# Kernel optimization log

Measured on AMD Instinct MI355X. Metric: run time of the kernel, lower is better.

Reference implementation:

```python
import jax, jax.numpy as jnp
import numpy as np

B, N, T, IN_DIM, OUT_DIM = 16, 500, 12, 2, 2
H, D, K, NH, NBLOCKS, T_OUT, GDEP = 64, 64, 10, 24, 2, 12, 2
H2 = 2 * H


def setup_inputs():
    key = jax.random.key(0)
    ks = iter(jax.random.split(key, 64))

    def rn(shape, s=1.0):
        return jax.random.normal(next(ks), shape, dtype=jnp.float32) * s

    def z(*shape):
        return jnp.zeros(shape, jnp.float32)

    sI = 1.0 / np.sqrt(IN_DIM)
    sH = 1.0 / np.sqrt(H)
    sH2 = 1.0 / np.sqrt(H2)
    sD = 1.0 / np.sqrt(D)
    adj = jax.random.uniform(next(ks), (N, N), dtype=jnp.float32)
    inp = {
        'x': rn((B, N, T, IN_DIM)),
        'weather': rn((B, T, 4)),
        'geo_adj': adj / adj.sum(1, keepdims=True),
        'fcx_W': rn((IN_DIM, H), sI), 'fcx_b': z(H),
        'env_cb': rn((K, D)), 'nodes_cb': rn((N, D)),
        'w_v': rn((D, K), sD), 'w_k': rn((D, D), sD), 'w_q': rn((D, D), sD),
        'core_W': rn((H, H * H), sH), 'core_b': z(H * H),
        'tcnN_Win': rn((K, H2, H2), sH2), 'tcnN_bin': z(K, H2),
        'tcnN_Wf': rn((K, NBLOCKS, 2, H2, H2), sH2), 'tcnN_bf': z(K, NBLOCKS, H2),
        'tcnN_Wg': rn((K, NBLOCKS, 2, H2, H2), sH2), 'tcnN_bg': z(K, NBLOCKS, H2),
        'tcnN_Wout': rn((K, H2, H), sH2), 'tcnN_bout': z(K, H),
        'tcnP_Win': rn((K, H2, H2), sH2), 'tcnP_bin': z(K, H2),
        'tcnP_Wf': rn((K, NBLOCKS, 2, H2, H2), sH2), 'tcnP_bf': z(K, NBLOCKS, H2),
        'tcnP_Wg': rn((K, NBLOCKS, 2, H2, H2), sH2), 'tcnP_bg': z(K, NBLOCKS, H2),
        'tcnP_Wout': rn((K, H2, H), sH2), 'tcnP_bout': z(K, H),
        'bn1_g': jnp.ones((H,), jnp.float32), 'bn1_b': z(H),
        'bnP_g': jnp.ones((H,), jnp.float32), 'bnP_b': z(H),
        'gcn1_W': rn((H, H), sH), 'gcn1_b': z(H),
        'gcn2_W': rn((H, H), sH), 'gcn2_b': z(H),
        'gcnp_W': rn((H, H), sH), 'gcnp_b': z(H),
        'nv_p1': rn((2 * NH, H)), 'nv_p2': rn((N, H)), 'nv_p3': rn((N, H)),
        'nv_pk': rn((H, H, H), sH),
        'out_W1': rn((T_OUT, H, 100), sH), 'out_b1': z(T_OUT, 100),
        'out_W2': rn((T_OUT, 100, OUT_DIM), 0.1), 'out_b2': z(T_OUT, OUT_DIM),
        't_pos': jax.random.randint(next(ks), (B, T, 2), 0, 7),
        'ind': jax.random.randint(next(ks), (B, T, 2), 0, 7),
    }
    return inp


def _tstep_emb(t, dim):
    half = dim // 2
    freqs = jnp.exp(-jnp.log(10000.0) * jnp.arange(half, dtype=jnp.float32) / half)
    a = t.astype(jnp.float32)[:, None] * freqs[None]
    return jnp.concatenate([jnp.cos(a), jnp.sin(a)], -1)


def _conv2(h, W, b, d):
    # causal kernel-2 dilated conv over time: h [B,N,T,C], W [2,C,Co] -> [B,N,T-d,Co]
    return (jnp.einsum('bntc,co->bnto', h[:, :, :-d], W[0])
            + jnp.einsum('bntc,co->bnto', h[:, :, d:], W[1]) + b)


def _tcn(xin, Win, bin_, Wf, bf, Wg, bg, Wout, bout):
    # gated dilated TCN (Graph-WaveNet style), per node over time
    h = jnp.einsum('bntc,co->bnto', xin, Win) + bin_
    for l in range(Wf.shape[0]):
        d = 2 ** l
        f = jnp.tanh(_conv2(h, Wf[l], bf[l], d))
        g = jax.nn.sigmoid(_conv2(h, Wg[l], bg[l], d))
        h = f * g + h[:, :, d:, :]
    return jnp.einsum('bntc,ch->bnth', h, Wout) + bout


def _bn(h, g, b):
    # BatchNorm1d over channels, stats over (batch, nodes); training mode
    mu = h.mean((0, 1))
    var = h.var((0, 1))
    return g * (h - mu) * jax.lax.rsqrt(var + 1e-5) + b


def _gcn(h, adj, W, b):
    # multi-hop diffusion: sum_{k=0..GDEP} A^k h, then linear
    eq = 'nm,bmh->bnh' if adj.ndim == 2 else 'bnm,bmh->bnh'
    acc, zt = h, h
    for _ in range(GDEP):
        zt = jnp.einsum(eq, adj, zt)
        acc = acc + zt
    return jnp.einsum('bnh,ho->bno', acc, W) + b


def _forward(x, weather, geo_adj, fcx_W, fcx_b, env_cb, nodes_cb, w_v, w_k, w_q,
             core_W, core_b,
             tcnN_Win, tcnN_bin, tcnN_Wf, tcnN_bf, tcnN_Wg, tcnN_bg, tcnN_Wout, tcnN_bout,
             tcnP_Win, tcnP_bin, tcnP_Wf, tcnP_bf, tcnP_Wg, tcnP_bg, tcnP_Wout, tcnP_bout,
             bn1_g, bn1_b, bnP_g, bnP_b, gcn1_W, gcn1_b, gcn2_W, gcn2_b, gcnp_W, gcnp_b,
             nv_p1, nv_p2, nv_p3, nv_pk, out_W1, out_b1, out_W2, out_b2, t_pos, ind):
    scale = 1.0 / jnp.sqrt(jnp.float32(D))
    ind_p = jnp.where(ind[:, :, 0] <= 4, ind[:, :, 1], NH - 1 + ind[:, :, 1])
    tp = jnp.where(t_pos[:, :, 0] <= 4, t_pos[:, :, 1], NH - 1 + t_pos[:, :, 1])
    t_emb = _tstep_emb(tp.reshape(-1), H).reshape(B, T, H)

    # codebook attention -> hard cluster assignment (gumbel softmax, straight-through)
    mat_v = env_cb @ w_v
    mat_k = env_cb @ w_k
    mat_q = nodes_cb @ w_q
    scores = jax.nn.softmax((mat_q @ mat_k.T) * scale, axis=1)
    logits = scores @ mat_v                                   # [N,K]
    gn = jax.random.gumbel(jax.random.key(42), logits.shape, dtype=logits.dtype)
    y_soft = jax.nn.softmax(logits + gn, axis=1)
    hard = jax.nn.one_hot(jnp.argmax(y_soft, axis=1), K, dtype=y_soft.dtype)
    mask = y_soft + jax.lax.stop_gradient(hard - y_soft)      # [N,K] one-hot fwd

    x_emb = jnp.einsum('bnti,ih->bnth', x, fcx_W) + fcx_b
    total_x = jnp.concatenate(
        [x_emb, jnp.broadcast_to(t_emb[:, None], (B, N, T, H))], -1)  # [B,N,T,2H]

    unbias = jnp.zeros((B, N, H), total_x.dtype)
    h_prev = jnp.zeros((B, N, H), total_x.dtype)
    for i in range(K):  # small fixed cluster count
        m = mask[:, i]
        xm = total_x * m[None, :, None, None]
        hn = _tcn(xm[:, :, 1:], tcnN_Win[i], tcnN_bin[i], tcnN_Wf[i], tcnN_bf[i],
                  tcnN_Wg[i], tcnN_bg[i], tcnN_Wout[i], tcnN_bout[i])[:, :, 0, :]
        hp = _tcn(xm[:, :, :-1], tcnP_Win[i], tcnP_bin[i], tcnP_Wf[i], tcnP_bf[i],
                  tcnP_Wg[i], tcnP_bg[i], tcnP_Wout[i], tcnP_bout[i])[:, :, 0, :]
        unbias = unbias + m[None, :, None] * hn
        h_prev = h_prev + m[None, :, None] * hp

    unbias = _bn(unbias, bn1_g, bn1_b)
    h_prev = _bn(h_prev, bnP_g, bnP_b)

    h1 = _gcn(h_prev, geo_adj, gcn1_W, gcn1_b)
    core = (t_emb[:, T - 1] @ core_W + core_b).reshape(B, H, H)
    causal = jax.nn.softmax(jnp.einsum('bnh,bhk,bmk->bnm', unbias, core, h_prev), axis=-1)
    h2 = _gcn(unbias, causal, gcn2_W, gcn2_b)

    te = nv_p1[ind_p[:, -(T - 1)]]                            # [B,H]
    adp = jnp.einsum('ai,ijk->ajk', te, nv_pk)
    adp = jnp.einsum('bj,ajk->abk', nv_p2, adp)
    adp = jnp.einsum('ck,abk->abc', nv_p3, adp)
    adp = jax.nn.softmax(jax.nn.relu(adp), axis=2)            # [B,N,N]
    h3 = _gcn(unbias, adp, gcnp_W, gcnp_b)

    cur_h = h1 + h2 + h3
    hmid = jax.nn.elu(jnp.einsum('bnh,thf->bntf', cur_h, out_W1) + out_b1)
    return jnp.einsum('bntf,tfo->bnto', hmid, out_W2) + out_b2  # [B,N,T_OUT,OUT_DIM]


def reference(x, weather, geo_adj, fcx_W, fcx_b, env_cb, nodes_cb, w_v, w_k, w_q,
              core_W, core_b,
              tcnN_Win, tcnN_bin, tcnN_Wf, tcnN_bf, tcnN_Wg, tcnN_bg, tcnN_Wout, tcnN_bout,
              tcnP_Win, tcnP_bin, tcnP_Wf, tcnP_bf, tcnP_Wg, tcnP_bg, tcnP_Wout, tcnP_bout,
              bn1_g, bn1_b, bnP_g, bnP_b, gcn1_W, gcn1_b, gcn2_W, gcn2_b, gcnp_W, gcnp_b,
              nv_p1, nv_p2, nv_p3, nv_pk, out_W1, out_b1, out_W2, out_b2, t_pos, ind):
    return _forward(x, weather, geo_adj, fcx_W, fcx_b, env_cb, nodes_cb, w_v, w_k, w_q,
                    core_W, core_b,
                    tcnN_Win, tcnN_bin, tcnN_Wf, tcnN_bf, tcnN_Wg, tcnN_bg, tcnN_Wout, tcnN_bout,
                    tcnP_Win, tcnP_bin, tcnP_Wf, tcnP_bf, tcnP_Wg, tcnP_bg, tcnP_Wout, tcnP_bout,
                    bn1_g, bn1_b, bnP_g, bnP_b, gcn1_W, gcn1_b, gcn2_W, gcn2_b, gcnp_W, gcnp_b,
                    nv_p1, nv_p2, nv_p3, nv_pk, out_W1, out_b1, out_W2, out_b2, t_pos, ind)
```

## Files before the change

### kernel.cpp

```cpp
#include <hip/hip_runtime.h>
#include <hip/hip_bf16.h>
#include <math.h>

#define B_ 16
#define N_ 500
#define T_ 12
#define K_ 10
#define NROWS (B_*N_)
#define TROWS 6

__device__ __forceinline__ unsigned rotl32(unsigned v, int r){ return (v<<r)|(v>>(32-r)); }

__device__ __forceinline__ void threefry2x32(unsigned k0, unsigned k1,
                                             unsigned c0, unsigned c1,
                                             unsigned &o0, unsigned &o1){
  unsigned ks2 = k0 ^ k1 ^ 0x1BD11BDAu;
  unsigned x0 = c0 + k0, x1 = c1 + k1;
#define TF_R(r) { x0 += x1; x1 = rotl32(x1,(r)); x1 ^= x0; }
  TF_R(13) TF_R(15) TF_R(26) TF_R(6)
  x0 += k1;  x1 += ks2 + 1u;
  TF_R(17) TF_R(29) TF_R(16) TF_R(24)
  x0 += ks2; x1 += k0 + 2u;
  TF_R(13) TF_R(15) TF_R(26) TF_R(6)
  x0 += k0;  x1 += k1 + 3u;
  TF_R(17) TF_R(29) TF_R(16) TF_R(24)
  x0 += k1;  x1 += ks2 + 4u;
  TF_R(13) TF_R(15) TF_R(26) TF_R(6)
  x0 += ks2; x1 += k0 + 5u;
#undef TF_R
  o0 = x0; o1 = x1;
}

__device__ __forceinline__ float gumbel_at(unsigned idx){
  unsigned b0, b1;
  threefry2x32(0u, 42u, 0u, idx, b0, b1);
  unsigned bits = b0 ^ b1;
  float u = __uint_as_float((bits >> 9) | 0x3f800000u) - 1.0f;
  u = fmaxf(u, 1.17549435e-38f);
  return -logf(-logf(u));
}

__global__ __launch_bounds__(256) void k_matq(const float* __restrict__ nodes_cb,
                                              const float* __restrict__ w_q,
                                              float* __restrict__ matq){
  int idx = blockIdx.x*256 + threadIdx.x;
  if (idx >= N_*64) return;
  int n = idx >> 6, d = idx & 63;
  float a = 0.f;
  for (int c = 0; c < 64; ++c) a += nodes_cb[n*64+c] * w_q[c*64+d];
  matq[idx] = a;
}

__global__ __launch_bounds__(256) void k_route(const float* __restrict__ env_cb,
                                               const float* __restrict__ w_v,
                                               const float* __restrict__ w_k,
                                               const float* __restrict__ matq,
                                               int* __restrict__ node_list,
                                               int* __restrict__ off){
  __shared__ float smk[K_*64];
  __shared__ float smv[K_*K_];
  __shared__ int sroute[N_];
  int tid = threadIdx.x;
  for (int idx = tid; idx < K_*64; idx += 256){
    int kk = idx >> 6, d = idx & 63;
    float a = 0.f;
    for (int c = 0; c < 64; ++c) a += env_cb[kk*64+c] * w_k[c*64+d];
    smk[idx] = a;
  }
  for (int idx = tid; idx < K_*K_; idx += 256){
    int kk = idx / K_, j = idx % K_;
    float a = 0.f;
    for (int c = 0; c < 64; ++c) a += env_cb[kk*64+c] * w_v[c*K_+j];
    smv[idx] = a;
  }
  __syncthreads();
  for (int n = tid; n < N_; n += 256){
    float s[K_];
    float mx = -1e30f;
    for (int j = 0; j < K_; ++j){
      float a = 0.f;
      for (int d = 0; d < 64; ++d) a += matq[n*64+d]*smk[j*64+d];
      s[j] = a * 0.125f;
      mx = fmaxf(mx, s[j]);
    }
    float sum = 0.f;
    for (int j = 0; j < K_; ++j){ s[j] = expf(s[j]-mx); sum += s[j]; }
    float inv = 1.f/sum;
    int best = 0; float bestv = -1e30f;
    for (int j2 = 0; j2 < K_; ++j2){
      float lg = 0.f;
      for (int j = 0; j < K_; ++j) lg += s[j]*inv*smv[j*K_+j2];
      float tot = lg + gumbel_at((unsigned)(n*K_+j2));
      if (tot > bestv){ bestv = tot; best = j2; }
    }
    sroute[n] = best;
  }
  __syncthreads();
  if (tid == 0){
    int cnt[K_]; for (int j=0;j<K_;++j) cnt[j]=0;
    for (int n=0;n<N_;++n) cnt[sroute[n]]++;
    int acc=0;
    for (int j=0;j<K_;++j){ off[j]=acc; acc+=cnt[j]; }
    off[K_]=acc;
    int pos[K_]; for (int j=0;j<K_;++j) pos[j]=off[j];
    for (int n=0;n<N_;++n) node_list[pos[sroute[n]]++] = n;
  }
}

__global__ void k_temb(const int* __restrict__ t_pos, float* __restrict__ temb){
  int tid = threadIdx.x;
  if (tid >= B_*T_) return;
  int b = tid / T_, t = tid % T_;
  int p0 = t_pos[(b*T_+t)*2+0], p1 = t_pos[(b*T_+t)*2+1];
  float tp = (float)((p0 <= 4) ? p1 : 23 + p1);
  float c0 = -logf(10000.f)/32.f;
  for (int j = 0; j < 32; ++j){
    float a = tp * expf(c0 * (float)j);
    temb[(b*T_+t)*64 + j]      = cosf(a);
    temb[(b*T_+t)*64 + 32 + j] = sinf(a);
  }
}

__global__ __launch_bounds__(256) void k_core(const float* __restrict__ temb,
                                              const float* __restrict__ core_W,
                                              const float* __restrict__ core_b,
                                              float* __restrict__ core_f){
  int idx = blockIdx.x*256 + threadIdx.x;
  if (idx >= B_*4096) return;
  int b = idx >> 12, c = idx & 4095;
  const float* te = temb + (b*T_ + 11)*64;
  float a = core_b[c];
  for (int h = 0; h < 64; ++h) a += te[h] * core_W[h*4096 + c];
  core_f[idx] = a;
}

__global__ __launch_bounds__(256) void k_tmp1(const int* __restrict__ ind,
                                              const float* __restrict__ nv_p1,
                                              const float* __restrict__ nv_pk,
                                              float* __restrict__ tmp1){
  int idx = blockIdx.x*256 + threadIdx.x;
  if (idx >= B_*4096) return;
  int b = idx >> 12, c = idx & 4095;
  int i0 = ind[(b*T_+1)*2+0], i1 = ind[(b*T_+1)*2+1];
  int row = (i0 <= 4) ? i1 : 23 + i1;
  const float* te = nv_p1 + row*64;
  float a = 0.f;
  for (int h = 0; h < 64; ++h) a += te[h] * nv_pk[h*4096 + c];
  tmp1[idx] = a;
}

__global__ __launch_bounds__(256) void k_tcn(
    const float* __restrict__ x,
    const float* __restrict__ fcx_W, const float* __restrict__ fcx_b,
    const float* __restrict__ temb,
    const int* __restrict__ node_list, const int* __restrict__ off,
    const float* __restrict__ WinN, const float* __restrict__ binN,
    const float* __restrict__ WfN,  const float* __restrict__ bfN,
    const float* __restrict__ WgN,  const float* __restrict__ bgN,
    const float* __restrict__ WoutN,const float* __restrict__ boutN,
    const float* __restrict__ WinP, const float* __restrict__ binP,
    const float* __restrict__ WfP,  const float* __restrict__ bfP,
    const float* __restrict__ WgP,  const float* __restrict__ bgP,
    const float* __restrict__ WoutP,const float* __restrict__ boutP,
    float* __restrict__ out_unb, float* __restrict__ out_hpr)
{
  int slot = blockIdx.x;
  int k = slot >> 1;
  int path = slot & 1;
  int cnt = off[k+1] - off[k];
  int rows = cnt * 16;
  int r0 = blockIdx.y * TROWS;
  if (r0 >= rows) return;

  const float* Win  = (path ? WinP  : WinN)  + k*16384;
  const float* bin  = (path ? binP  : binN)  + k*128;
  const float* Wf   = (path ? WfP   : WfN)   + k*4*16384;
  const float* bf_  = (path ? bfP   : bfN)   + k*2*128;
  const float* Wg   = (path ? WgP   : WgN)   + k*4*16384;
  const float* bg_  = (path ? bgP   : bgN)   + k*2*128;
  const float* Wout = (path ? WoutP : WoutN) + k*8192;
  const float* bout = (path ? boutP : boutN) + k*64;
  float* outb = path ? out_hpr : out_unb;
  int t0 = path ? 0 : 1;

  __shared__ __align__(16) float sIn[TROWS*512];
  __shared__ __align__(16) float sH0[TROWS*512];
  __shared__ __align__(16) float sH1[TROWS*256];
  __shared__ __align__(16) float sH2[TROWS*128];
  __shared__ int rowBN[TROWS];
  __shared__ int rowB[TROWS];

  int tid = threadIdx.x;
  if (tid < TROWS){
    int r = r0 + tid;
    if (r < rows){
      int node = node_list[off[k] + (r >> 4)];
      int b = r & 15;
      rowBN[tid] = b*N_ + node;
      rowB[tid]  = b;
    } else { rowBN[tid] = -1; rowB[tid] = 0; }
  }
  __syncthreads();

  for (int i = 0; i < TROWS; ++i){
    int rb = rowBN[i], b = rowB[i];
    for (int c2 = tid; c2 < 512; c2 += 256){
      int t = (c2 >> 7) + t0, c = c2 & 127;
      float v = 0.f;
      if (rb >= 0){
        if (c < 64){
          const float* xp = x + (rb*T_ + t)*2;
          v = xp[0]*fcx_W[c] + xp[1]*fcx_W[64+c] + fcx_b[c];
        } else {
          v = temb[(b*T_ + t)*64 + (c-64)];
        }
      }
      sIn[i*512 + c2] = v;
    }
  }
  __syncthreads();

  {
    int oc = (tid & 63)*2;
    int jg = (tid >> 6)*6;
    float a0[6], a1[6];
    #pragma unroll
    for (int j=0;j<6;++j){ a0[j]=0.f; a1[j]=0.f; }
    for (int c = 0; c < 128; c += 4){
      float2 w0 = *(const float2*)(Win + (c+0)*128 + oc);
      float2 w1 = *(const float2*)(Win + (c+1)*128 + oc);
      float2 w2 = *(const float2*)(Win + (c+2)*128 + oc);
      float2 w3 = *(const float2*)(Win + (c+3)*128 + oc);
      #pragma unroll
      for (int j=0;j<6;++j){
        float4 xv = *(const float4*)&sIn[(jg+j)*128 + c];
        a0[j] += xv.x*w0.x + xv.y*w1.x + xv.z*w2.x + xv.w*w3.x;
        a1[j] += xv.x*w0.y + xv.y*w1.y + xv.z*w2.y + xv.w*w3.y;
      }
    }
    float b0v = bin[oc], b1v = bin[oc+1];
    #pragma unroll
    for (int j=0;j<6;++j){
      sH0[(jg+j)*128 + oc]   = a0[j] + b0v;
      sH0[(jg+j)*128 + oc+1] = a1[j] + b1v;
    }
  }
  __syncthreads();

  {
    int o = tid & 127;
    int jg = (tid >> 7)*6;
    float af[6], ag[6];
    #pragma unroll
    for (int j=0;j<6;++j){ af[j]=0.f; ag[j]=0.f; }
    for (int c = 0; c < 128; c += 4){
      float f00=Wf[(c+0)*128+o], f01=Wf[(c+1)*128+o], f02=Wf[(c+2)*128+o], f03=Wf[(c+3)*128+o];
      float f10=Wf[16384+(c+0)*128+o], f11=Wf[16384+(c+1)*128+o], f12=Wf[16384+(c+2)*128+o], f13=Wf[16384+(c+3)*128+o];
      float g00=Wg[(c+0)*128+o], g01=Wg[(c+1)*128+o], g02=Wg[(c+2)*128+o], g03=Wg[(c+3)*128+o];
      float g10=Wg[16384+(c+0)*128+o], g11=Wg[16384+(c+1)*128+o], g12=Wg[16384+(c+2)*128+o], g13=Wg[16384+(c+3)*128+o];
      #pragma unroll
      for (int jj=0;jj<6;++jj){
        int j = jg + jj;
        int i = j >> 1, ti = j & 1;
        float4 xa = *(const float4*)&sH0[(i*4+ti*2  )*128 + c];
        float4 xb = *(const float4*)&sH0[(i*4+ti*2+1)*128 + c];
        af[jj] += xa.x*f00 + xa.y*f01 + xa.z*f02 + xa.w*f03
                + xb.x*f10 + xb.y*f11 + xb.z*f12 + xb.w*f13;
        ag[jj] += xa.x*g00 + xa.y*g01 + xa.z*g02 + xa.w*g03
                + xb.x*g10 + xb.y*g11 + xb.z*g12 + xb.w*g13;
      }
    }
    float bfv = bf_[o], bgv = bg_[o];
    #pragma unroll
    for (int jj=0;jj<6;++jj){
      int j = jg + jj;
      int i = j >> 1, ti = j & 1;
      float f = tanhf(af[jj] + bfv);
      float g = 1.f/(1.f + expf(-(ag[jj] + bgv)));
      sH1[j*128 + o] = f*g + sH0[(i*4 + ti*2 + 1)*128 + o];
    }
  }
  __syncthreads();

  {
    int o = tid & 127;
    int ig = (tid >> 7)*3;
    const float* Wf1 = Wf + 2*16384;
    const float* Wg1 = Wg + 2*16384;
    float af[3], ag[3];
    #pragma unroll
    for (int i=0;i<3;++i){ af[i]=0.f; ag[i]=0.f; }
    for (int c = 0; c < 128; c += 4){
      float f00=Wf1[(c+0)*128+o], f01=Wf1[(c+1)*128+o], f02=Wf1[(c+2)*128+o], f03=Wf1[(c+3)*128+o];
      float f10=Wf1[16384+(c+0)*128+o], f11=Wf1[16384+(c+1)*128+o], f12=Wf1[16384+(c+2)*128+o], f13=Wf1[16384+(c+3)*128+o];
      float g00=Wg1[(c+0)*128+o], g01=Wg1[(c+1)*128+o], g02=Wg1[(c+2)*128+o], g03=Wg1[(c+3)*128+o];
      float g10=Wg1[16384+(c+0)*128+o], g11=Wg1[16384+(c+1)*128+o], g12=Wg1[16384+(c+2)*128+o], g13=Wg1[16384+(c+3)*128+o];
      #pragma unroll
      for (int ii=0;ii<3;++ii){
        int i = ig + ii;
        float4 xa = *(const float4*)&sH1[(i*2+0)*128 + c];
        float4 xb = *(const float4*)&sH1[(i*2+1)*128 + c];
        af[ii] += xa.x*f00 + xa.y*f01 + xa.z*f02 + xa.w*f03
                + xb.x*f10 + xb.y*f11 + xb.z*f12 + xb.w*f13;
        ag[ii] += xa.x*g00 + xa.y*g01 + xa.z*g02 + xa.w*g03
                + xb.x*g10 + xb.y*g11 + xb.z*g12 + xb.w*g13;
      }
    }
    float bfv = bf_[128+o], bgv = bg_[128+o];
    #pragma unroll
    for (int ii=0;ii<3;++ii){
      int i = ig + ii;
      float f = tanhf(af[ii] + bfv);
      float g = 1.f/(1.f + expf(-(ag[ii] + bgv)));
      sH2[i*128 + o] = f*g + sH1[(i*2+1)*128 + o];
    }
  }
  __syncthreads();

  {
    int o6 = tid & 63, grp = tid >> 6;
    #pragma unroll
    for (int ii=0; ii<2; ++ii){
      int i = grp*2 + ii;
      if (i >= TROWS) continue;
      float acc = 0.f;
      for (int c = 0; c < 128; c += 4){
        float w0=Wout[(c+0)*64+o6], w1=Wout[(c+1)*64+o6],
              w2=Wout[(c+2)*64+o6], w3=Wout[(c+3)*64+o6];
        float4 xv = *(const float4*)&sH2[i*128 + c];
        acc += xv.x*w0 + xv.y*w1 + xv.z*w2 + xv.w*w3;
      }
      if (rowBN[i] >= 0) outb[rowBN[i]*64 + o6] = acc + bout[o6];
    }
  }
}

__global__ __launch_bounds__(256) void k_bnstats(const float* __restrict__ unb,
                                                 const float* __restrict__ hpr,
                                                 float* __restrict__ stats){
  int bid = blockIdx.x;
  int tensor = bid >> 6, c = bid & 63;
  const float* buf = tensor ? hpr : unb;
  float s1 = 0.f, s2 = 0.f;
  for (int r = threadIdx.x; r < NROWS; r += 256){
    float v = buf[r*64 + c];
    s1 += v; s2 += v*v;
  }
  __shared__ float r1[256], r2[256];
  r1[threadIdx.x]=s1; r2[threadIdx.x]=s2;
  __syncthreads();
  for (int s=128; s>0; s>>=1){
    if (threadIdx.x < s){ r1[threadIdx.x]+=r1[threadIdx.x+s]; r2[threadIdx.x]+=r2[threadIdx.x+s]; }
    __syncthreads();
  }
  if (threadIdx.x==0){
    float mean = r1[0]/(float)NROWS;
    float var  = r2[0]/(float)NROWS - mean*mean;
    stats[tensor*128 + c]      = mean;
    stats[tensor*128 + 64 + c] = rsqrtf(var + 1e-5f);
  }
}

__global__ __launch_bounds__(256) void k_bnapply(float* __restrict__ unb, float* __restrict__ hpr,
                                                 const float* __restrict__ stats,
                                                 const float* __restrict__ g1, const float* __restrict__ be1,
                                                 const float* __restrict__ gP, const float* __restrict__ beP){
  int idx = blockIdx.x*256 + threadIdx.x;
  if (idx >= 2*NROWS*64) return;
  int tensor = idx >= NROWS*64;
  int local = idx - tensor*NROWS*64;
  int c = local & 63;
  float* buf = tensor ? hpr : unb;
  float mean = stats[tensor*128+c], rstd = stats[tensor*128+64+c];
  float g = tensor ? gP[c] : g1[c];
  float bb = tensor ? beP[c] : be1[c];
  buf[local] = g * (buf[local]-mean) * rstd + bb;
}

template<int AMODE, int RELU, int FINAL, int ADD>
__global__ __launch_bounds__(256) void k_attn(
    const float* __restrict__ geo,
    const float* __restrict__ Qf, const float* __restrict__ Qb,
    const float* __restrict__ M,
    const float* __restrict__ Keysf, const float* __restrict__ Keysb,
    const float* __restrict__ X,
    const float* __restrict__ X0, const float* __restrict__ Z1,
    const float* __restrict__ Wg, const float* __restrict__ bg,
    float* __restrict__ cur, float* __restrict__ Y)
{
  __shared__ __align__(16) float vbuf[16][68];
  __shared__ __align__(16) float mb[2][64][68];
  __shared__ __align__(16) float sbuf[16][516];
  __shared__ float red[16][17];
  __shared__ float rowm[16], rowinv[16];

  int b = blockIdx.y, n0 = blockIdx.x*16;
  int tid = threadIdx.x;
  int nl = tid >> 4, ml = tid & 15;
  int n = n0 + nl;
  float rr[16];

  if (AMODE == 0){
    for (int idx = tid; idx < 16*512; idx += 256){
      int r = idx >> 9, m = idx & 511;
      int nn = n0 + r;
      sbuf[r][m] = (nn < N_ && m < N_) ? geo[nn*N_+m] : 0.f;
    }
    __syncthreads();
  } else {
    for (int idx = tid; idx < 1024; idx += 256){
      int r = idx >> 6, kk = idx & 63;
      int nn = n0 + r;
      float q = 0.f;
      if (nn < N_) q = (AMODE == 1) ? Qf[(b*N_+nn)*64+kk] : Qb[nn*64+kk];
      vbuf[r][kk] = q;
    }
    for (int idx = tid; idx < 4096; idx += 256){
      int kk = idx >> 6, c = idx & 63;
      mb[0][kk][c] = M[b*4096 + idx];
    }
    __syncthreads();
    float4 v4 = {0.f,0.f,0.f,0.f};
    for (int kk = 0; kk < 64; ++kk){
      float q = vbuf[nl][kk];
      float4 m4 = *(const float4*)&mb[0][kk][ml*4];
      v4.x += q*m4.x; v4.y += q*m4.y; v4.z += q*m4.z; v4.w += q*m4.w;
    }
    __syncthreads();
    *(float4*)&vbuf[nl][ml*4] = v4;

    #pragma unroll
    for (int ii=0; ii<16; ++ii){
      int idx = tid + ii*256;
      int mm = idx >> 6, kk = idx & 63;
      rr[ii] = (AMODE == 1) ? Keysf[(b*N_+mm)*64+kk] : Keysb[mm*64+kk];
    }
    #pragma unroll
    for (int ii=0; ii<16; ++ii){
      int idx = tid + ii*256;
      mb[0][idx >> 6][idx & 63] = rr[ii];
    }
    __syncthreads();
    for (int ci = 0; ci < 8; ++ci){
      int m0 = ci*64;
      int cb = ci & 1, nb = (ci+1) & 1;
      if (ci < 7){
        #pragma unroll
        for (int ii=0; ii<16; ++ii){
          int idx = tid + ii*256;
          int mm = idx >> 6, kk = idx & 63;
          int m = m0 + 64 + mm;
          rr[ii] = 0.f;
          if (m < N_) rr[ii] = (AMODE == 1) ? Keysf[(b*N_+m)*64+kk] : Keysb[m*64+kk];
        }
      }
      {
        float s0=0.f, s1=0.f, s2=0.f, s3=0.f;
        for (int kk = 0; kk < 64; kk += 4){
          float4 qv  = *(const float4*)&vbuf[nl][kk];
          float4 k0v = *(const float4*)&mb[cb][ml   ][kk];
          float4 k1v = *(const float4*)&mb[cb][ml+16][kk];
          float4 k2v = *(const float4*)&mb[cb][ml+32][kk];
          float4 k3v = *(const float4*)&mb[cb][ml+48][kk];
          s0 += qv.x*k0v.x + qv.y*k0v.y + qv.z*k0v.z + qv.w*k0v.w;
          s1 += qv.x*k1v.x + qv.y*k1v.y + qv.z*k1v.z + qv.w*k1v.w;
          s2 += qv.x*k2v.x + qv.y*k2v.y + qv.z*k2v.z + qv.w*k2v.w;
          s3 += qv.x*k3v.x + qv.y*k3v.y + qv.z*k3v.z + qv.w*k3v.w;
        }
        sbuf[nl][m0+ml   ] = s0;
        sbuf[nl][m0+ml+16] = s1;
        sbuf[nl][m0+ml+32] = s2;
        sbuf[nl][m0+ml+48] = s3;
      }
      if (ci < 7){
        #pragma unroll
        for (int ii=0; ii<16; ++ii){
          int idx = tid + ii*256;
          mb[nb][idx >> 6][idx & 63] = rr[ii];
        }
      }
      __syncthreads();
    }
    float lmax = -1e30f;
    for (int m = ml; m < N_; m += 16){
      float v = sbuf[nl][m];
      if (RELU) v = fmaxf(v, 0.f);
      lmax = fmaxf(lmax, v);
    }
    red[nl][ml] = lmax;
    __syncthreads();
    if (ml == 0){
      float mx = red[nl][0];
      for (int j=1;j<16;++j) mx = fmaxf(mx, red[nl][j]);
      rowm[nl] = mx;
    }
    __syncthreads();
    float mx = rowm[nl];
    float lsum = 0.f;
    for (int m = ml; m < N_; m += 16){
      float v = sbuf[nl][m];
      if (RELU) v = fmaxf(v, 0.f);
      lsum += expf(v - mx);
    }
    red[nl][ml] = lsum;
    __syncthreads();
    if (ml == 0){
      float s = 0.f;
      for (int j=0;j<16;++j) s += red[nl][j];
      rowinv[nl] = 1.f/s;
    }
    __syncthreads();
    float inv = rowinv[nl];
    for (int m = ml; m < 512; m += 16){
      float p = 0.f;
      if (m < N_){
        float v = sbuf[nl][m];
        if (RELU) v = fmaxf(v, 0.f);
        p = expf(v - mx)*inv;
      }
      sbuf[nl][m] = p;
    }
    __syncthreads();
  }

  float4 acc4 = {0.f,0.f,0.f,0.f};
  #pragma unroll
  for (int ii=0; ii<16; ++ii){
    int idx = tid + ii*256;
    int mm = idx >> 6, kk = idx & 63;
    rr[ii] = X[(b*N_+mm)*64+kk];
  }
  #pragma unroll
  for (int ii=0; ii<16; ++ii){
    int idx = tid + ii*256;
    mb[0][idx >> 6][idx & 63] = rr[ii];
  }
  __syncthreads();
  for (int ci = 0; ci < 8; ++ci){
    int m0 = ci*64;
    int cb = ci & 1, nb = (ci+1) & 1;
    if (ci < 7){
      #pragma unroll
      for (int ii=0; ii<16; ++ii){
        int idx = tid + ii*256;
        int mm = idx >> 6, kk = idx & 63;
        int m = m0 + 64 + mm;
        rr[ii] = (m < N_) ? X[(b*N_+m)*64+kk] : 0.f;
      }
    }
    for (int mm = 0; mm < 64; mm += 4){
      float4 pv  = *(const float4*)&sbuf[nl][m0+mm];
      float4 x0v = *(const float4*)&mb[cb][mm+0][ml*4];
      float4 x1v = *(const float4*)&mb[cb][mm+1][ml*4];
      float4 x2v = *(const float4*)&mb[cb][mm+2][ml*4];
      float4 x3v = *(const float4*)&mb[cb][mm+3][ml*4];
      acc4.x += pv.x*x0v.x + pv.y*x1v.x + pv.z*x2v.x + pv.w*x3v.x;
      acc4.y += pv.x*x0v.y + pv.y*x1v.y + pv.z*x2v.y + pv.w*x3v.y;
      acc4.z += pv.x*x0v.z + pv.y*x1v.z + pv.z*x2v.z + pv.w*x3v.z;
      acc4.w += pv.x*x0v.w + pv.y*x1v.w + pv.z*x2v.w + pv.w*x3v.w;
    }
    if (ci < 7){
      #pragma unroll
      for (int ii=0; ii<16; ++ii){
        int idx = tid + ii*256;
        mb[nb][idx >> 6][idx & 63] = rr[ii];
      }
    }
    __syncthreads();
  }

  if (!FINAL){
    if (n < N_) *(float4*)&Y[(b*N_+n)*64 + ml*4] = acc4;
    return;
  }

  {
    int row = b*N_ + n;
    float4 sv = {0.f,0.f,0.f,0.f};
    if (n < N_){
      float4 x0v = *(const float4*)&X0[row*64 + ml*4];
      float4 z1v = *(const float4*)&Z1[row*64 + ml*4];
      sv.x = acc4.x + x0v.x + z1v.x;
      sv.y = acc4.y + x0v.y + z1v.y;
      sv.z = acc4.z + x0v.z + z1v.z;
      sv.w = acc4.w + x0v.w + z1v.w;
    }
    *(float4*)&vbuf[nl][ml*4] = sv;
    for (int idx = tid; idx < 4096; idx += 256){
      int kk = idx >> 6, c = idx & 63;
      mb[0][kk][c] = Wg[idx];
    }
    __syncthreads();
    float4 o4 = {0.f,0.f,0.f,0.f};
    for (int kk = 0; kk < 64; ++kk){
      float s = vbuf[nl][kk];
      float4 w4 = *(const float4*)&mb[0][kk][ml*4];
      o4.x += s*w4.x; o4.y += s*w4.y; o4.z += s*w4.z; o4.w += s*w4.w;
    }
    if (n < N_){
      float4 bv = *(const float4*)&bg[ml*4];
      float4 val;
      val.x = o4.x + bv.x; val.y = o4.y + bv.y;
      val.z = o4.z + bv.z; val.w = o4.w + bv.w;
      if (ADD){
        float4 old = *(const float4*)&cur[row*64 + ml*4];
        val.x += old.x; val.y += old.y; val.z += old.z; val.w += old.w;
      }
      *(float4*)&cur[row*64 + ml*4] = val;
    }
  }
}

__global__ __launch_bounds__(128) void k_out(const float* __restrict__ cur,
                                             const float* __restrict__ W1, const float* __restrict__ bb1,
                                             const float* __restrict__ W2, const float* __restrict__ bb2,
                                             float* __restrict__ out){
  __shared__ float ch[4][64];
  __shared__ float hid[4*1200];
  int tid = threadIdx.x;
  int rbase = blockIdx.x*4;
  for (int idx = tid; idx < 256; idx += 128){
    int r = idx >> 6, h = idx & 63;
    ch[r][h] = cur[(rbase+r)*64 + h];
  }
  __syncthreads();
  for (int job = tid; job < 1200; job += 128){
    int t = job / 100, f = job - t*100;
    float a0 = bb1[t*100+f], a1 = a0, a2 = a0, a3 = a0;
    for (int h = 0; h < 64; ++h){
      float w = W1[(t*64+h)*100 + f];
      a0 += ch[0][h]*w; a1 += ch[1][h]*w; a2 += ch[2][h]*w; a3 += ch[3][h]*w;
    }
    hid[0*1200+job] = (a0 > 0.f) ? a0 : expm1f(a0);
    hid[1*1200+job] = (a1 > 0.f) ? a1 : expm1f(a1);
    hid[2*1200+job] = (a2 > 0.f) ? a2 : expm1f(a2);
    hid[3*1200+job] = (a3 > 0.f) ? a3 : expm1f(a3);
  }
  __syncthreads();
  if (tid < 96){
    int r = tid / 24, rem = tid % 24;
    int t = rem >> 1, o = rem & 1;
    float a = bb2[t*2+o];
    const float* hp = hid + r*1200 + t*100;
    for (int f = 0; f < 100; ++f) a += hp[f] * W2[(t*100+f)*2+o];
    out[(rbase+r)*24 + t*2+o] = a;
  }
}

extern "C" void kernel_launch(void* const* d_in, const int* in_sizes, int n_in,
                              void* d_out, int out_size, void* d_ws, size_t ws_size,
                              hipStream_t stream)
{
  const float* x        = (const float*)d_in[0];
  const float* geo      = (const float*)d_in[2];
  const float* fcx_W    = (const float*)d_in[3];
  const float* fcx_b    = (const float*)d_in[4];
  const float* env_cb   = (const float*)d_in[5];
  const float* nodes_cb = (const float*)d_in[6];
  const float* w_v      = (const float*)d_in[7];
  const float* w_k      = (const float*)d_in[8];
  const float* w_q      = (const float*)d_in[9];
  const float* core_W   = (const float*)d_in[10];
  const float* core_b   = (const float*)d_in[11];
  const float* tN_Win   = (const float*)d_in[12];
  const float* tN_bin   = (const float*)d_in[13];
  const float* tN_Wf    = (const float*)d_in[14];
  const float* tN_bf    = (const float*)d_in[15];
  const float* tN_Wg    = (const float*)d_in[16];
  const float* tN_bg    = (const float*)d_in[17];
  const float* tN_Wout  = (const float*)d_in[18];
  const float* tN_bout  = (const float*)d_in[19];
  const float* tP_Win   = (const float*)d_in[20];
  const float* tP_bin   = (const float*)d_in[21];
  const float* tP_Wf    = (const float*)d_in[22];
  const float* tP_bf    = (const float*)d_in[23];
  const float* tP_Wg    = (const float*)d_in[24];
  const float* tP_bg    = (const float*)d_in[25];
  const float* tP_Wout  = (const float*)d_in[26];
  const float* tP_bout  = (const float*)d_in[27];
  const float* bn1_g    = (const float*)d_in[28];
  const float* bn1_b    = (const float*)d_in[29];
  const float* bnP_g    = (const float*)d_in[30];
  const float* bnP_b    = (const float*)d_in[31];
  const float* gcn1_W   = (const float*)d_in[32];
  const float* gcn1_b   = (const float*)d_in[33];
  const float* gcn2_W   = (const float*)d_in[34];
  const float* gcn2_b   = (const float*)d_in[35];
  const float* gcnp_W   = (const float*)d_in[36];
  const float* gcnp_b   = (const float*)d_in[37];
  const float* nv_p1    = (const float*)d_in[38];
  const float* nv_p2    = (const float*)d_in[39];
  const float* nv_p3    = (const float*)d_in[40];
  const float* nv_pk    = (const float*)d_in[41];
  const float* out_W1   = (const float*)d_in[42];
  const float* out_b1   = (const float*)d_in[43];
  const float* out_W2   = (const float*)d_in[44];
  const float* out_b2   = (const float*)d_in[45];
  const int*   t_pos    = (const int*)d_in[46];
  const int*   ind      = (const int*)d_in[47];

  int* node_list = (int*)d_ws;
  int* off       = node_list + 512;
  float* F = (float*)((char*)d_ws + 4096);
  float* temb   = F + 0;
  float* core_f = F + 12288;
  float* tmp1   = F + 77824;
  float* stats  = F + 143360;
  float* matq   = F + 143616;
  float* unb    = F + 175616;
  float* hpr    = F + 687616;
  float* cur    = F + 1199616;
  float* zt1    = F + 1711616;

  k_matq <<<dim3(125), dim3(256), 0, stream>>>(nodes_cb, w_q, matq);
  k_route<<<dim3(1),   dim3(256), 0, stream>>>(env_cb, w_v, w_k, matq, node_list, off);
  k_temb <<<dim3(1),   dim3(192), 0, stream>>>(t_pos, temb);
  k_core <<<dim3(256), dim3(256), 0, stream>>>(temb, core_W, core_b, core_f);
  k_tcn  <<<dim3(20, 334), dim3(256), 0, stream>>>(x, fcx_W, fcx_b, temb, node_list, off,
      tN_Win, tN_bin, tN_Wf, tN_bf, tN_Wg, tN_bg, tN_Wout, tN_bout,
      tP_Win, tP_bin, tP_Wf, tP_bf, tP_Wg, tP_bg, tP_Wout, tP_bout,
      unb, hpr);
  k_bnstats<<<dim3(128), dim3(256), 0, stream>>>(unb, hpr, stats);
  k_bnapply<<<dim3(4000),dim3(256), 0, stream>>>(unb, hpr, stats, bn1_g, bn1_b, bnP_g, bnP_b);

  dim3 ag(32, 16);
  k_attn<0,0,0,0><<<ag, 256, 0, stream>>>(geo, nullptr,nullptr,nullptr, nullptr,nullptr,
                                 hpr, nullptr,nullptr, nullptr,nullptr, nullptr, zt1);
  k_attn<0,0,1,0><<<ag, 256, 0, stream>>>(geo, nullptr,nullptr,nullptr, nullptr,nullptr,
                                 zt1, hpr, zt1, gcn1_W, gcn1_b, cur, nullptr);
  k_attn<1,0,0,0><<<ag, 256, 0, stream>>>(nullptr, unb,nullptr, core_f, hpr,nullptr,
                                 unb, nullptr,nullptr, nullptr,nullptr, nullptr, zt1);
  k_attn<1,0,1,1><<<ag, 256, 0, stream>>>(nullptr, unb,nullptr, core_f, hpr,nullptr,
                                 zt1, unb, zt1, gcn2_W, gcn2_b, cur, nullptr);
  k_tmp1<<<dim3(256), dim3(256), 0, stream>>>(ind, nv_p1, nv_pk, tmp1);
  k_attn<2,1,0,0><<<ag, 256, 0, stream>>>(nullptr, nullptr,nv_p2, tmp1, nullptr,nv_p3,
                                 unb, nullptr,nullptr, nullptr,nullptr, nullptr, zt1);
  k_attn<2,1,1,1><<<ag, 256, 0, stream>>>(nullptr, nullptr,nv_p2, tmp1, nullptr,nv_p3,
                                 zt1, unb, zt1, gcnp_W, gcnp_b, cur, nullptr);
  k_out<<<dim3(2000), dim3(128), 0, stream>>>(cur, out_W1, out_b1, out_W2, out_b2, (float*)d_out);
}
```

Measured before the change: 1.017 ms.

## Convert attention kernel to flash-style online softmax with 8-row tiles

The attention kernel no longer materialises a full 16x512 score row buffer in shared memory. It computes scores per 64-column chunk and applies an online softmax (running max and sum, wave-level shuffle reductions), accumulating P·X on the fly with keys and X streamed together. Rows per block drop from 16 to 8 and the grid doubles. The aim is lower LDS use for higher occupancy and fewer passes, but K/X tiles are now loaded twice as often across blocks and extra barriers are added per chunk.

```diff
diff --git a/kernel.cpp b/kernel.cpp
--- a/kernel.cpp
+++ b/kernel.cpp
@@ -388,225 +388,183 @@
     const float* __restrict__ Wg, const float* __restrict__ bg,
     float* __restrict__ cur, float* __restrict__ Y)
 {
-  __shared__ __align__(16) float vbuf[16][68];
-  __shared__ __align__(16) float mb[2][64][68];
-  __shared__ __align__(16) float sbuf[16][516];
-  __shared__ float red[16][17];
-  __shared__ float rowm[16], rowinv[16];
-
-  int b = blockIdx.y, n0 = blockIdx.x*16;
+  __shared__ __align__(16) float kbuf[64][65];
+  __shared__ __align__(16) float xbuf[64][64];
+  __shared__ __align__(16) float vbuf[8][64];
+  __shared__ __align__(16) float pbuf[8][64];
+
+  int b = blockIdx.y, n0 = blockIdx.x*8;
   int tid = threadIdx.x;
-  int nl = tid >> 4, ml = tid & 15;
+  int nl = tid >> 5, ml = tid & 31;
   int n = n0 + nl;
-  float rr[16];
-
-  if (AMODE == 0){
-    for (int idx = tid; idx < 16*512; idx += 256){
-      int r = idx >> 9, m = idx & 511;
-      int nn = n0 + r;
-      sbuf[r][m] = (nn < N_ && m < N_) ? geo[nn*N_+m] : 0.f;
-    }
-    __syncthreads();
-  } else {
-    for (int idx = tid; idx < 1024; idx += 256){
+  float rrK[16], rrX[16], rrA[2];
+
+  if (AMODE != 0){
+    for (int idx = tid; idx < 512; idx += 256){
       int r = idx >> 6, kk = idx & 63;
       int nn = n0 + r;
       float q = 0.f;
       if (nn < N_) q = (AMODE == 1) ? Qf[(b*N_+nn)*64+kk] : Qb[nn*64+kk];
-      vbuf[r][kk] = q;
-    }
-    for (int idx = tid; idx < 4096; idx += 256){
-      int kk = idx >> 6, c = idx & 63;
-      mb[0][kk][c] = M[b*4096 + idx];
-    }
+      pbuf[r][kk] = q;
+    }
+    for (int idx = tid; idx < 4096; idx += 256)
+      kbuf[idx>>6][idx&63] = M[b*4096 + idx];
     __syncthreads();
-    float4 v4 = {0.f,0.f,0.f,0.f};
+    float vx = 0.f, vy = 0.f;
     for (int kk = 0; kk < 64; ++kk){
-      float q = vbuf[nl][kk];
-      float4 m4 = *(const float4*)&mb[0][kk][ml*4];
-      v4.x += q*m4.x; v4.y += q*m4.y; v4.z += q*m4.z; v4.w += q*m4.w;
+      float q = pbuf[nl][kk];
+      float2 m2 = *(const float2*)&kbuf[kk][ml*2];
+      vx += q*m2.x; vy += q*m2.y;
     }
     __syncthreads();
-    *(float4*)&vbuf[nl][ml*4] = v4;
-
-    #pragma unroll
-    for (int ii=0; ii<16; ++ii){
+    vbuf[nl][ml*2]   = vx;
+    vbuf[nl][ml*2+1] = vy;
+  }
+  {
+    if (AMODE != 0) __syncthreads();
+    #pragma unroll
+    for (int ii = 0; ii < 16; ++ii){
       int idx = tid + ii*256;
       int mm = idx >> 6, kk = idx & 63;
-      rr[ii] = (AMODE == 1) ? Keysf[(b*N_+mm)*64+kk] : Keysb[mm*64+kk];
-    }
-    #pragma unroll
-    for (int ii=0; ii<16; ++ii){
-      int idx = tid + ii*256;
-      mb[0][idx >> 6][idx & 63] = rr[ii];
+      if (AMODE != 0)
+        kbuf[mm][kk] = (AMODE == 1) ? Keysf[(b*N_+mm)*64+kk] : Keysb[mm*64+kk];
+      xbuf[mm][kk] = X[(b*N_+mm)*64+kk];
+    }
+    if (AMODE == 0){
+      #pragma unroll
+      for (int ii = 0; ii < 2; ++ii){
+        int idx = tid + ii*256;
+        int r = idx >> 6, mm = idx & 63;
+        int nn = n0 + r;
+        pbuf[r][mm] = (nn < N_) ? geo[nn*N_ + mm] : 0.f;
+      }
     }
     __syncthreads();
-    for (int ci = 0; ci < 8; ++ci){
-      int m0 = ci*64;
-      int cb = ci & 1, nb = (ci+1) & 1;
-      if (ci < 7){
-        #pragma unroll
-        for (int ii=0; ii<16; ++ii){
-          int idx = tid + ii*256;
-          int mm = idx >> 6, kk = idx & 63;
-          int m = m0 + 64 + mm;
-          rr[ii] = 0.f;
-          if (m < N_) rr[ii] = (AMODE == 1) ? Keysf[(b*N_+m)*64+kk] : Keysb[m*64+kk];
-        }
-      }
-      {
-        float s0=0.f, s1=0.f, s2=0.f, s3=0.f;
-        for (int kk = 0; kk < 64; kk += 4){
-          float4 qv  = *(const float4*)&vbuf[nl][kk];
-          float4 k0v = *(const float4*)&mb[cb][ml   ][kk];
-          float4 k1v = *(const float4*)&mb[cb][ml+16][kk];
-          float4 k2v = *(const float4*)&mb[cb][ml+32][kk];
-          float4 k3v = *(const float4*)&mb[cb][ml+48][kk];
-          s0 += qv.x*k0v.x + qv.y*k0v.y + qv.z*k0v.z + qv.w*k0v.w;
-          s1 += qv.x*k1v.x + qv.y*k1v.y + qv.z*k1v.z + qv.w*k1v.w;
-          s2 += qv.x*k2v.x + qv.y*k2v.y + qv.z*k2v.z + qv.w*k2v.w;
-          s3 += qv.x*k3v.x + qv.y*k3v.y + qv.z*k3v.z + qv.w*k3v.w;
-        }
-        sbuf[nl][m0+ml   ] = s0;
-        sbuf[nl][m0+ml+16] = s1;
-        sbuf[nl][m0+ml+32] = s2;
-        sbuf[nl][m0+ml+48] = s3;
-      }
-      if (ci < 7){
-        #pragma unroll
-        for (int ii=0; ii<16; ++ii){
-          int idx = tid + ii*256;
-          mb[nb][idx >> 6][idx & 63] = rr[ii];
-        }
-      }
-      __syncthreads();
-    }
-    float lmax = -1e30f;
-    for (int m = ml; m < N_; m += 16){
-      float v = sbuf[nl][m];
-      if (RELU) v = fmaxf(v, 0.f);
-      lmax = fmaxf(lmax, v);
-    }
-    red[nl][ml] = lmax;
-    __syncthreads();
-    if (ml == 0){
-      float mx = red[nl][0];
-      for (int j=1;j<16;++j) mx = fmaxf(mx, red[nl][j]);
-      rowm[nl] = mx;
-    }
-    __syncthreads();
-    float mx = rowm[nl];
-    float lsum = 0.f;
-    for (int m = ml; m < N_; m += 16){
-      float v = sbuf[nl][m];
-      if (RELU) v = fmaxf(v, 0.f);
-      lsum += expf(v - mx);
-    }
-    red[nl][ml] = lsum;
-    __syncthreads();
-    if (ml == 0){
-      float s = 0.f;
-      for (int j=0;j<16;++j) s += red[nl][j];
-      rowinv[nl] = 1.f/s;
-    }
-    __syncthreads();
-    float inv = rowinv[nl];
-    for (int m = ml; m < 512; m += 16){
-      float p = 0.f;
-      if (m < N_){
-        float v = sbuf[nl][m];
-        if (RELU) v = fmaxf(v, 0.f);
-        p = expf(v - mx)*inv;
-      }
-      sbuf[nl][m] = p;
-    }
-    __syncthreads();
-  }
-
-  float4 acc4 = {0.f,0.f,0.f,0.f};
-  #pragma unroll
-  for (int ii=0; ii<16; ++ii){
-    int idx = tid + ii*256;
-    int mm = idx >> 6, kk = idx & 63;
-    rr[ii] = X[(b*N_+mm)*64+kk];
-  }
-  #pragma unroll
-  for (int ii=0; ii<16; ++ii){
-    int idx = tid + ii*256;
-    mb[0][idx >> 6][idx & 63] = rr[ii];
-  }
-  __syncthreads();
+  }
+
+  float m_run = -1e30f, l_run = 0.f;
+  float accx = 0.f, accy = 0.f;
+
   for (int ci = 0; ci < 8; ++ci){
     int m0 = ci*64;
-    int cb = ci & 1, nb = (ci+1) & 1;
     if (ci < 7){
       #pragma unroll
       for (int ii=0; ii<16; ++ii){
         int idx = tid + ii*256;
         int mm = idx >> 6, kk = idx & 63;
         int m = m0 + 64 + mm;
-        rr[ii] = (m < N_) ? X[(b*N_+m)*64+kk] : 0.f;
-      }
-    }
+        if (AMODE != 0)
+          rrK[ii] = (m < N_) ? ((AMODE == 1) ? Keysf[(b*N_+m)*64+kk] : Keysb[m*64+kk]) : 0.f;
+        rrX[ii] = (m < N_) ? X[(b*N_+m)*64+kk] : 0.f;
+      }
+      if (AMODE == 0){
+        #pragma unroll
+        for (int ii=0; ii<2; ++ii){
+          int idx = tid + ii*256;
+          int r = idx >> 6, mm = idx & 63;
+          int nn = n0 + r, m = m0 + 64 + mm;
+          rrA[ii] = (nn < N_ && m < N_) ? geo[nn*N_ + m] : 0.f;
+        }
+      }
+    }
+    if (AMODE != 0){
+      float s0 = 0.f, s1 = 0.f;
+      for (int kk = 0; kk < 64; kk += 4){
+        float4 qv = *(const float4*)&vbuf[nl][kk];
+        float4 k0 = *(const float4*)&kbuf[ml   ][kk];
+        float4 k1 = *(const float4*)&kbuf[ml+32][kk];
+        s0 += qv.x*k0.x + qv.y*k0.y + qv.z*k0.z + qv.w*k0.w;
+        s1 += qv.x*k1.x + qv.y*k1.y + qv.z*k1.z + qv.w*k1.w;
+      }
+      float v0 = (m0 + ml      < N_) ? (RELU ? fmaxf(s0, 0.f) : s0) : -1e30f;
+      float v1 = (m0 + ml + 32 < N_) ? (RELU ? fmaxf(s1, 0.f) : s1) : -1e30f;
+      float cmax = fmaxf(v0, v1);
+      #pragma unroll
+      for (int msk = 1; msk < 32; msk <<= 1) cmax = fmaxf(cmax, __shfl_xor(cmax, msk, 32));
+      float mnew = fmaxf(m_run, cmax);
+      float scale = expf(m_run - mnew);
+      float p0 = expf(v0 - mnew);
+      float p1 = expf(v1 - mnew);
+      float lc = p0 + p1;
+      #pragma unroll
+      for (int msk = 1; msk < 32; msk <<= 1) lc += __shfl_xor(lc, msk, 32);
+      l_run = l_run*scale + lc;
+      m_run = mnew;
+      accx *= scale; accy *= scale;
+      pbuf[nl][ml]    = p0;
+      pbuf[nl][ml+32] = p1;
+    }
+    __syncthreads();
     for (int mm = 0; mm < 64; mm += 4){
-      float4 pv  = *(const float4*)&sbuf[nl][m0+mm];
-      float4 x0v = *(const float4*)&mb[cb][mm+0][ml*4];
-      float4 x1v = *(const float4*)&mb[cb][mm+1][ml*4];
-      float4 x2v = *(const float4*)&mb[cb][mm+2][ml*4];
-      float4 x3v = *(const float4*)&mb[cb][mm+3][ml*4];
-      acc4.x += pv.x*x0v.x + pv.y*x1v.x + pv.z*x2v.x + pv.w*x3v.x;
-      acc4.y += pv.x*x0v.y + pv.y*x1v.y + pv.z*x2v.y + pv.w*x3v.y;
-      acc4.z += pv.x*x0v.z + pv.y*x1v.z + pv.z*x2v.z + pv.w*x3v.z;
-      acc4.w += pv.x*x0v.w + pv.y*x1v.w + pv.z*x2v.w + pv.w*x3v.w;
-    }
+      float4 pv = *(const float4*)&pbuf[nl][mm];
+      float2 x0 = *(const float2*)&xbuf[mm+0][ml*2];
+      float2 x1 = *(const float2*)&xbuf[mm+1][ml*2];
+      float2 x2 = *(const float2*)&xbuf[mm+2][ml*2];
+      float2 x3 = *(const float2*)&xbuf[mm+3][ml*2];
+      accx += pv.x*x0.x + pv.y*x1.x + pv.z*x2.x + pv.w*x3.x;
+      accy += pv.x*x0.y + pv.y*x1.y + pv.z*x2.y + pv.w*x3.y;
+    }
+    __syncthreads();
     if (ci < 7){
       #pragma unroll
       for (int ii=0; ii<16; ++ii){
         int idx = tid + ii*256;
-        mb[nb][idx >> 6][idx & 63] = rr[ii];
-      }
-    }
-    __syncthreads();
+        int mm = idx >> 6, kk = idx & 63;
+        if (AMODE != 0) kbuf[mm][kk] = rrK[ii];
+        xbuf[mm][kk] = rrX[ii];
+      }
+      if (AMODE == 0){
+        #pragma unroll
+        for (int ii=0; ii<2; ++ii){
+          int idx = tid + ii*256;
+          pbuf[idx>>6][idx&63] = rrA[ii];
+        }
+      }
+      __syncthreads();
+    }
+  }
+  if (AMODE != 0){
+    float inv = 1.f / l_run;
+    accx *= inv; accy *= inv;
   }
 
   if (!FINAL){
-    if (n < N_) *(float4*)&Y[(b*N_+n)*64 + ml*4] = acc4;
+    if (n < N_){
+      float2 o2; o2.x = accx; o2.y = accy;
+      *(float2*)&Y[(b*N_+n)*64 + ml*2] = o2;
+    }
     return;
   }
 
   {
     int row = b*N_ + n;
-    float4 sv = {0.f,0.f,0.f,0.f};
+    float svx = 0.f, svy = 0.f;
     if (n < N_){
-      float4 x0v = *(const float4*)&X0[row*64 + ml*4];
-      float4 z1v = *(const float4*)&Z1[row*64 + ml*4];
-      sv.x = acc4.x + x0v.x + z1v.x;
-      sv.y = acc4.y + x0v.y + z1v.y;
-      sv.z = acc4.z + x0v.z + z1v.z;
-      sv.w = acc4.w + x0v.w + z1v.w;
-    }
-    *(float4*)&vbuf[nl][ml*4] = sv;
-    for (int idx = tid; idx < 4096; idx += 256){
-      int kk = idx >> 6, c = idx & 63;
-      mb[0][kk][c] = Wg[idx];
-    }
+      float2 x0v = *(const float2*)&X0[row*64 + ml*2];
+      float2 z1v = *(const float2*)&Z1[row*64 + ml*2];
+      svx = accx + x0v.x + z1v.x;
+      svy = accy + x0v.y + z1v.y;
+    }
+    vbuf[nl][ml*2]   = svx;
+    vbuf[nl][ml*2+1] = svy;
+    for (int idx = tid; idx < 4096; idx += 256)
+      kbuf[idx>>6][idx&63] = Wg[idx];
     __syncthreads();
-    float4 o4 = {0.f,0.f,0.f,0.f};
+    float ox = 0.f, oy = 0.f;
     for (int kk = 0; kk < 64; ++kk){
       float s = vbuf[nl][kk];
-      float4 w4 = *(const float4*)&mb[0][kk][ml*4];
-      o4.x += s*w4.x; o4.y += s*w4.y; o4.z += s*w4.z; o4.w += s*w4.w;
+      float2 w2 = *(const float2*)&kbuf[kk][ml*2];
+      ox += s*w2.x; oy += s*w2.y;
     }
     if (n < N_){
-      float4 bv = *(const float4*)&bg[ml*4];
-      float4 val;
-      val.x = o4.x + bv.x; val.y = o4.y + bv.y;
-      val.z = o4.z + bv.z; val.w = o4.w + bv.w;
+      float2 bv = *(const float2*)&bg[ml*2];
+      float vx = ox + bv.x, vy = oy + bv.y;
       if (ADD){
-        float4 old = *(const float4*)&cur[row*64 + ml*4];
-        val.x += old.x; val.y += old.y; val.z += old.z; val.w += old.w;
-      }
-      *(float4*)&cur[row*64 + ml*4] = val;
+        float2 old = *(const float2*)&cur[row*64 + ml*2];
+        vx += old.x; vy += old.y;
+      }
+      float2 o2; o2.x = vx; o2.y = vy;
+      *(float2*)&cur[row*64 + ml*2] = o2;
     }
   }
 }
@@ -723,7 +681,7 @@
   k_bnstats<<<dim3(128), dim3(256), 0, stream>>>(unb, hpr, stats);
   k_bnapply<<<dim3(4000),dim3(256), 0, stream>>>(unb, hpr, stats, bn1_g, bn1_b, bnP_g, bnP_b);
 
-  dim3 ag(32, 16);
+  dim3 ag(64, 16);
   k_attn<0,0,0,0><<<ag, 256, 0, stream>>>(geo, nullptr,nullptr,nullptr, nullptr,nullptr,
                                  hpr, nullptr,nullptr, nullptr,nullptr, nullptr, zt1);
   k_attn<0,0,1,0><<<ag, 256, 0, stream>>>(geo, nullptr,nullptr,nullptr, nullptr,nullptr,
```

Measured after the change: 969.6 us. -4.7%, faster.
